# Optimization experiments

Hardware: AMD Instinct MI355X
Metric: run time of the kernel (lower is better)

Reference implementation:

```python
import jax, jax.numpy as jnp
import numpy as np
import math

B, L, D, H = 16, 512, 128, 8


def setup_inputs() -> dict:
    key = jax.random.key(0)
    ks = jax.random.split(key, 10)
    xavier = lambda k, shp: jax.random.normal(k, shp, jnp.float32) * math.sqrt(2.0 / (shp[0] + shp[1]))
    inp = {
        "x": jax.random.normal(ks[0], (B, L, D), jnp.float32),
        "W_q": xavier(ks[1], (H * D, D)),
        "b_q": jnp.zeros((H * D,), jnp.float32),
        "W_k": xavier(ks[2], (H * D, D)),
        "b_k": jnp.zeros((H * D,), jnp.float32),
        "W_v": xavier(ks[3], (H * D, D)),
        "b_v": jnp.zeros((H * D,), jnp.float32),
        "W_o": xavier(ks[4], (D, H * D)),
        "b_o": jnp.zeros((D,), jnp.float32),
        "pad_mask": jax.random.randint(ks[5], (B, L, L), 0, 2).astype(bool),
        "batch_size": B,
        "max_len": L,
    }
    return inp


def reference(x, W_q, b_q, W_k, b_k, W_v, b_v, W_o, b_o, pad_mask, batch_size, max_len):
    # project: [B, L, D] -> [B, L, H*D] -> head-major [H*B, L, D]
    def proj(W, b):
        y = jnp.einsum('bld,ed->ble', x, W) + b          # [B, L, H*D]
        y = y.reshape(batch_size, max_len, H, D)
        return y.transpose(2, 0, 1, 3).reshape(H * batch_size, max_len, D)

    q = proj(W_q, b_q)
    k = proj(W_k, b_k)
    v = proj(W_v, b_v)

    scores = jnp.einsum('nqd,nkd->nqk', q, k)            # [H*B, L, L]
    mask = jnp.tile(pad_mask, (H, 1, 1))                 # repeat(n_heads,1,1)
    # faithful quirk: mask BEFORE scaling, softmax over QUERY axis (dim=1)
    scores = jnp.where(mask, -1e9, scores) / math.sqrt(D)
    attn = jax.nn.softmax(scores, axis=1)
    att = jnp.einsum('nqk,nkd->nqd', attn, v)            # [H*B, L, D]
    # faithful quirk: torch .view from (H*B, L, D) to (B, L, H*D)
    att = att.reshape(batch_size, max_len, H * D)
    out = jnp.einsum('ble,de->bld', att, W_o) + b_o      # [B, L, D]
    return out
```

## Files before the change

### kernel.cpp

```cpp
#include <hip/hip_runtime.h>

#define B_  16
#define L_  512
#define D_  128
#define H_  8
#define HD_ 1024
#define NH_ 128
#define M_  8192

typedef unsigned short u16;
typedef __attribute__((ext_vector_type(8))) short s16x8;
typedef __attribute__((ext_vector_type(4))) float f32x4;

__device__ __forceinline__ float bf2f(u16 u) {
    union { unsigned u; float f; } x; x.u = ((unsigned)u) << 16; return x.f;
}
__device__ __forceinline__ u16 f2bf(float f) {
    unsigned u = __float_as_uint(f);
    return (u16)((u + 0x7FFFu + ((u >> 16) & 1u)) >> 16);
}

__device__ __forceinline__ void mfma_bt64(const u16* __restrict__ A, int lda,
                                          const u16* __restrict__ B, int ldb,
                                          int K, int lane, f32x4 acc[4][4]) {
    const int mr = lane & 15, quad = lane >> 4;
    for (int k0 = 0; k0 < K; k0 += 32) {
        s16x8 av[4], bv[4];
#pragma unroll
        for (int i = 0; i < 4; i++)
            av[i] = *(const s16x8*)(A + (size_t)(i * 16 + mr) * lda + k0 + quad * 8);
#pragma unroll
        for (int j = 0; j < 4; j++)
            bv[j] = *(const s16x8*)(B + (size_t)(j * 16 + mr) * ldb + k0 + quad * 8);
#pragma unroll
        for (int i = 0; i < 4; i++)
#pragma unroll
            for (int j = 0; j < 4; j++)
                acc[i][j] = __builtin_amdgcn_mfma_f32_16x16x32_bf16(av[i], bv[j], acc[i][j], 0, 0, 0);
    }
}

__global__ void k0_detect(const unsigned int* __restrict__ pad,
                          const unsigned int* __restrict__ xw,
                          int* __restrict__ flags) {
    __shared__ int sMask, sCnt;
    if (threadIdx.x == 0) { sMask = 0; sCnt = 0; }
    __syncthreads();
    int bad = 0;
#pragma unroll
    for (int i = 0; i < 4; i++) {
        unsigned u = pad[threadIdx.x * 4 + i];
        bad |= (u > 1u) ? 1 : 0;
    }
    int cnt = 0;
#pragma unroll
    for (int i = 0; i < 16; i++) {
        unsigned w = xw[threadIdx.x * 16 + i];
        unsigned e = (w >> 7) & 0xFFu;
        cnt += (e >= 100u && e <= 131u) ? 1 : 0;
    }
    if (bad) atomicOr(&sMask, 1);
    atomicAdd(&sCnt, cnt);
    __syncthreads();
    if (threadIdx.x == 0) {
        flags[0] = (sCnt > 2048) ? 1 : 0;
        flags[1] = sMask;
    }
}

#define PREP_TOT 1576064
__global__ __launch_bounds__(256) void kprep_conv(
    const void* x, const void* Wq, const void* bq, const void* Wk, const void* bk,
    const void* Wv, const void* bv, const void* Wo, const void* bo,
    const int* __restrict__ flags,
    u16* xb, u16* Wqb, u16* Wkb, u16* Wvb, u16* Wob,
    u16* bqb, u16* bkb, u16* bvb, u16* bob) {
    int gid = blockIdx.x * 256 + threadIdx.x;
    if (gid >= PREP_TOT) return;
    const int dt = flags[0];
    const void* src; u16* dst; int off;
    if      (gid < 1048576) { src = x;  dst = xb;  off = gid; }
    else if (gid < 1179648) { src = Wq; dst = Wqb; off = gid - 1048576; }
    else if (gid < 1310720) { src = Wk; dst = Wkb; off = gid - 1179648; }
    else if (gid < 1441792) { src = Wv; dst = Wvb; off = gid - 1310720; }
    else if (gid < 1572864) { src = Wo; dst = Wob; off = gid - 1441792; }
    else if (gid < 1573888) { src = bq; dst = bqb; off = gid - 1572864; }
    else if (gid < 1574912) { src = bk; dst = bkb; off = gid - 1573888; }
    else if (gid < 1575936) { src = bv; dst = bvb; off = gid - 1574912; }
    else                    { src = bo; dst = bob; off = gid - 1575936; }
    dst[off] = dt ? ((const u16*)src)[off] : f2bf(((const float*)src)[off]);
}

__global__ __launch_bounds__(256) void kprep_mask(const void* __restrict__ pad,
                                                  const int* __restrict__ flags,
                                                  unsigned* __restrict__ mb) {
    int w = blockIdx.x * 256 + threadIdx.x;
    size_t base = (size_t)w * 32;
    unsigned m = 0;
    if (flags[1]) {
        const unsigned char* p = (const unsigned char*)pad;
#pragma unroll
        for (int b = 0; b < 32; b++) m |= (p[base + b] ? 1u : 0u) << b;
    } else {
        const int* p = (const int*)pad;
#pragma unroll
        for (int b = 0; b < 32; b++) m |= (p[base + b] ? 1u : 0u) << b;
    }
    mb[w] = m;
}

__global__ __launch_bounds__(256) void k1_proj(
    const u16* __restrict__ xb,
    const u16* __restrict__ Wqb, const u16* __restrict__ Wkb, const u16* __restrict__ Wvb,
    const u16* __restrict__ bqb, const u16* __restrict__ bkb, const u16* __restrict__ bvb,
    u16* __restrict__ qb, u16* __restrict__ kb, u16* __restrict__ vtb) {
    const int h  = blockIdx.x;
    const int m0 = blockIdx.y * 128;
    const int z  = blockIdx.z;
    const u16* W    = (z == 0) ? Wqb : (z == 1) ? Wkb : Wvb;
    const u16* bias = (z == 0) ? bqb : (z == 1) ? bkb : bvb;

    const int lane = threadIdx.x & 63, wave = threadIdx.x >> 6;
    const int wr = wave >> 1, wc = wave & 1;
    const int mr = lane & 15, quad = lane >> 4;

    f32x4 acc[4][4];
#pragma unroll
    for (int i = 0; i < 4; i++)
#pragma unroll
        for (int j = 0; j < 4; j++) acc[i][j] = (f32x4){0.f, 0.f, 0.f, 0.f};

    mfma_bt64(xb + (size_t)(m0 + wr * 64) * D_, D_,
              W + (size_t)(h * 128 + wc * 64) * D_, D_, D_, lane, acc);

    __shared__ __align__(16) u16 T[128][144];
#pragma unroll
    for (int i = 0; i < 4; i++)
#pragma unroll
        for (int j = 0; j < 4; j++) {
            int col = wc * 64 + j * 16 + mr;
            float bv_ = bf2f(bias[h * 128 + col]);
#pragma unroll
            for (int r = 0; r < 4; r++)
                T[wr * 64 + i * 16 + quad * 4 + r][col] = f2bf(acc[i][j][r] + bv_);
        }
    __syncthreads();

    const int bb = m0 >> 9, l0 = m0 & 511;
    const int t = threadIdx.x;
    if (z < 2) {
        u16* out = z ? kb : qb;
        int row = t >> 1, c0 = (t & 1) * 64;
        u16* dst = out + ((size_t)(h * B_ + bb) * L_ + l0 + row) * D_ + c0;
#pragma unroll
        for (int c = 0; c < 64; c += 8)
            *(uint4*)(dst + c) = *(const uint4*)&T[row][c0 + c];
    } else {
        int d = t >> 1, lc0 = (t & 1) * 64;
        u16* dst = vtb + ((size_t)(h * B_ + bb) * D_ + d) * L_ + l0 + lc0;
#pragma unroll
        for (int c = 0; c < 64; c += 8) {
            u16 tmp[8];
#pragma unroll
            for (int s = 0; s < 8; s++) tmp[s] = T[lc0 + c + s][d];
            *(uint4*)(dst + c) = *(const uint4*)tmp;
        }
    }
}

__global__ __launch_bounds__(256) void k2_scores(
    const u16* __restrict__ qb, const u16* __restrict__ kb,
    const unsigned* __restrict__ mbits,
    u16* __restrict__ sb, float* __restrict__ linv) {
    const int k0g = blockIdx.x * 128;
    const int n   = blockIdx.y;
    const int bb  = n & (B_ - 1);
    const int lane = threadIdx.x & 63, wave = threadIdx.x >> 6;
    const int wr = wave >> 1, wc = wave & 1;
    const int mr = lane & 15, quad = lane >> 4;
    const float rs = 0.08838834764831845f;

    __shared__ __align__(16) u16 T[128][144];
    __shared__ float CS[2][128];

    const u16* Abase = qb + (size_t)n * L_ * D_;
    const u16* Bbase = kb + (size_t)n * L_ * D_ + (size_t)(k0g + wc * 64) * D_;

    float colsum[4] = {0.f, 0.f, 0.f, 0.f};
    for (int qt = 0; qt < 4; qt++) {
        f32x4 acc[4][4];
#pragma unroll
        for (int i = 0; i < 4; i++)
#pragma unroll
            for (int j = 0; j < 4; j++) acc[i][j] = (f32x4){0.f, 0.f, 0.f, 0.f};

        mfma_bt64(Abase + (size_t)(qt * 128 + wr * 64) * D_, D_, Bbase, D_, D_, lane, acc);

#pragma unroll
        for (int i = 0; i < 4; i++)
#pragma unroll
            for (int j = 0; j < 4; j++) {
                int kc = k0g + wc * 64 + j * 16 + mr;
#pragma unroll
                for (int r = 0; r < 4; r++) {
                    int ql = wr * 64 + i * 16 + quad * 4 + r;
                    int q  = qt * 128 + ql;
                    unsigned w = mbits[((size_t)(bb << 9) + q) * 16 + (kc >> 5)];
                    float s = ((w >> (kc & 31)) & 1u) ? -1e9f : acc[i][j][r];
                    float e = __expf(s * rs);
                    colsum[j] += e;
                    T[ql][wc * 64 + j * 16 + mr] = f2bf(e);
                }
            }
        __syncthreads();
        {
            int t = threadIdx.x, row = t >> 1, c0 = (t & 1) * 64;
            u16* dst = sb + ((size_t)n * L_ + qt * 128 + row) * L_ + k0g + c0;
#pragma unroll
            for (int c = 0; c < 64; c += 8)
                *(uint4*)(dst + c) = *(const uint4*)&T[row][c0 + c];
        }
        __syncthreads();
    }
#pragma unroll
    for (int j = 0; j < 4; j++) {
        colsum[j] += __shfl_xor(colsum[j], 16);
        colsum[j] += __shfl_xor(colsum[j], 32);
    }
    if (quad == 0) {
#pragma unroll
        for (int j = 0; j < 4; j++) CS[wr][wc * 64 + j * 16 + mr] = colsum[j];
    }
    __syncthreads();
    if (threadIdx.x < 128)
        linv[(size_t)n * L_ + k0g + threadIdx.x] =
            1.0f / (CS[0][threadIdx.x] + CS[1][threadIdx.x]);
}

__global__ __launch_bounds__(256) void k3_vscale(u16* __restrict__ vtb,
                                                 const float* __restrict__ linv) {
    int idx = blockIdx.x * 256 + threadIdx.x;
    int n = idx >> 13;
    int rem = idx & 8191;
    int d = rem >> 6;
    int kg = (rem & 63) << 3;
    u16* p = vtb + ((size_t)n * D_ + d) * L_ + kg;
    uint4 v = *(const uint4*)p;
    float lv[8];
    *(float4*)&lv[0] = *(const float4*)(linv + (size_t)n * L_ + kg);
    *(float4*)&lv[4] = *(const float4*)(linv + (size_t)n * L_ + kg + 4);
    u16* u = (u16*)&v;
#pragma unroll
    for (int s = 0; s < 8; s++) u[s] = f2bf(bf2f(u[s]) * lv[s]);
    *(uint4*)p = v;
}

__global__ __launch_bounds__(256) void k4_av(
    const u16* __restrict__ sb, const u16* __restrict__ vtb,
    u16* __restrict__ att) {
    const int q0 = blockIdx.x * 128;
    const int n  = blockIdx.y;
    const int lane = threadIdx.x & 63, wave = threadIdx.x >> 6;
    const int wr = wave >> 1, wc = wave & 1;
    const int mr = lane & 15, quad = lane >> 4;

    f32x4 acc[4][4];
#pragma unroll
    for (int i = 0; i < 4; i++)
#pragma unroll
        for (int j = 0; j < 4; j++) acc[i][j] = (f32x4){0.f, 0.f, 0.f, 0.f};

    mfma_bt64(sb + ((size_t)n * L_ + q0 + wr * 64) * L_, L_,
              vtb + ((size_t)n * D_ + wc * 64) * L_, L_, L_, lane, acc);

    __shared__ __align__(16) u16 T[128][144];
#pragma unroll
    for (int i = 0; i < 4; i++)
#pragma unroll
        for (int j = 0; j < 4; j++) {
            int col = wc * 64 + j * 16 + mr;
#pragma unroll
            for (int r = 0; r < 4; r++)
                T[wr * 64 + i * 16 + quad * 4 + r][col] = f2bf(acc[i][j][r]);
        }
    __syncthreads();
    int t = threadIdx.x, row = t >> 1, c0 = (t & 1) * 64;
    u16* dst = att + ((size_t)n * L_ + q0 + row) * D_ + c0;
#pragma unroll
    for (int c = 0; c < 64; c += 8)
        *(uint4*)(dst + c) = *(const uint4*)&T[row][c0 + c];
}

__global__ __launch_bounds__(128) void k5_out(
    const u16* __restrict__ att, const u16* __restrict__ Wob,
    const u16* __restrict__ bob, const int* __restrict__ flags,
    void* __restrict__ out) {
    const int dt = flags[0];
    const int m0 = blockIdx.x * 64;
    const int lane = threadIdx.x & 63, wc = threadIdx.x >> 6;
    const int mr = lane & 15, quad = lane >> 4;

    f32x4 acc[4][4];
#pragma unroll
    for (int i = 0; i < 4; i++)
#pragma unroll
        for (int j = 0; j < 4; j++) acc[i][j] = (f32x4){0.f, 0.f, 0.f, 0.f};

    mfma_bt64(att + (size_t)m0 * HD_, HD_,
              Wob + (size_t)(wc * 64) * HD_, HD_, HD_, lane, acc);

    __shared__ __align__(16) float Tf[64][132];
#pragma unroll
    for (int i = 0; i < 4; i++)
#pragma unroll
        for (int j = 0; j < 4; j++) {
            int col = wc * 64 + j * 16 + mr;
            float bv_ = bf2f(bob[col]);
#pragma unroll
            for (int r = 0; r < 4; r++)
                Tf[i * 16 + quad * 4 + r][col] = acc[i][j][r] + bv_;
        }
    __syncthreads();
    int t = threadIdx.x, row = t >> 1, c0 = (t & 1) * 64;
    size_t base = (size_t)(m0 + row) * D_ + c0;
    if (dt) {
        u16* o = (u16*)out;
#pragma unroll
        for (int c = 0; c < 64; c += 8) {
            u16 tmp[8];
#pragma unroll
            for (int s = 0; s < 8; s++) tmp[s] = f2bf(Tf[row][c0 + c + s]);
            *(uint4*)(o + base + c) = *(const uint4*)tmp;
        }
    } else {
        float* o = (float*)out;
#pragma unroll
        for (int c = 0; c < 64; c += 4)
            *(float4*)(o + base + c) = *(const float4*)&Tf[row][c0 + c];
    }
}

extern "C" void kernel_launch(void* const* d_in, const int* in_sizes, int n_in,
                              void* d_out, int out_size, void* d_ws, size_t ws_size,
                              hipStream_t stream) {
    (void)in_sizes; (void)n_in; (void)out_size; (void)ws_size;
    const void* x  = d_in[0];
    const void* Wq = d_in[1]; const void* bq = d_in[2];
    const void* Wk = d_in[3]; const void* bk = d_in[4];
    const void* Wv = d_in[5]; const void* bv = d_in[6];
    const void* Wo = d_in[7]; const void* bo = d_in[8];
    const void* pad = d_in[9];

    char* p = (char*)d_ws;
    auto alloc = [&](size_t bytes) { char* r = p; p += (bytes + 255) & ~(size_t)255; return r; };
    int*  flags = (int*)alloc(256);
    u16*  xb   = (u16*)alloc(2097152);
    u16*  Wqb  = (u16*)alloc(262144);
    u16*  Wkb  = (u16*)alloc(262144);
    u16*  Wvb  = (u16*)alloc(262144);
    u16*  Wob  = (u16*)alloc(262144);
    u16*  bqb  = (u16*)alloc(2048);
    u16*  bkb  = (u16*)alloc(2048);
    u16*  bvb  = (u16*)alloc(2048);
    u16*  bob  = (u16*)alloc(256);
    unsigned* mbits = (unsigned*)alloc(524288);
    float* linv = (float*)alloc(262144);
    u16*  qb   = (u16*)alloc(16777216);
    u16*  kb   = (u16*)alloc(16777216);
    u16*  vtb  = (u16*)alloc(16777216);
    u16*  sb   = (u16*)alloc(67108864);
    u16*  att  = qb;

    k0_detect<<<1, 256, 0, stream>>>((const unsigned*)pad, (const unsigned*)x, flags);
    kprep_conv<<<(PREP_TOT + 255) / 256, 256, 0, stream>>>(
        x, Wq, bq, Wk, bk, Wv, bv, Wo, bo, flags,
        xb, Wqb, Wkb, Wvb, Wob, bqb, bkb, bvb, bob);
    kprep_mask<<<512, 256, 0, stream>>>(pad, flags, mbits);
    k1_proj<<<dim3(8, 64, 3), 256, 0, stream>>>(
        xb, Wqb, Wkb, Wvb, bqb, bkb, bvb, qb, kb, vtb);
    k2_scores<<<dim3(4, NH_), 256, 0, stream>>>(qb, kb, mbits, sb, linv);
    k3_vscale<<<4096, 256, 0, stream>>>(vtb, linv);
    k4_av<<<dim3(4, NH_), 256, 0, stream>>>(sb, vtb, att);
    k5_out<<<128, 128, 0, stream>>>(att, Wob, bob, flags, d_out);
}
```

Before: 253.4 us.

## Fuse scores, normalization and AV into flash-style kernel with recompute

The score kernel is split into a column-sum pass that only computes softmax denominators, and a second kernel that recomputes QK^T, applies the mask and per-key normalization, and multiplies with V in LDS. This removes the 64MB bf16 score matrix round-trip and the separate V-scaling kernel. The cost is computing QK^T twice. The output projection is also split over the K dimension across two waves, with a 2D grid for more blocks, and mask words are staged in LDS.

```diff
diff --git a/kernel.cpp b/kernel.cpp
--- a/kernel.cpp
+++ b/kernel.cpp
@@ -133,7 +133,7 @@
     mfma_bt64(xb + (size_t)(m0 + wr * 64) * D_, D_,
               W + (size_t)(h * 128 + wc * 64) * D_, D_, D_, lane, acc);
 
-    __shared__ __align__(16) u16 T[128][144];
+    __shared__ __align__(16) u16 T[128][136];
 #pragma unroll
     for (int i = 0; i < 4; i++)
 #pragma unroll
@@ -168,11 +168,10 @@
     }
 }
 
-__global__ __launch_bounds__(256) void k2_scores(
+__global__ __launch_bounds__(256) void k2a_linv(
     const u16* __restrict__ qb, const u16* __restrict__ kb,
-    const unsigned* __restrict__ mbits,
-    u16* __restrict__ sb, float* __restrict__ linv) {
-    const int k0g = blockIdx.x * 128;
+    const unsigned* __restrict__ mbits, float* __restrict__ linv) {
+    const int kstrip = blockIdx.x * 128;
     const int n   = blockIdx.y;
     const int bb  = n & (B_ - 1);
     const int lane = threadIdx.x & 63, wave = threadIdx.x >> 6;
@@ -180,11 +179,18 @@
     const int mr = lane & 15, quad = lane >> 4;
     const float rs = 0.08838834764831845f;
 
-    __shared__ __align__(16) u16 T[128][144];
+    __shared__ unsigned mw[2048];
     __shared__ float CS[2][128];
+#pragma unroll
+    for (int s = 0; s < 8; s++) {
+        int idx = threadIdx.x * 8 + s;
+        int q = idx >> 2, lw = idx & 3;
+        mw[idx] = mbits[((size_t)(bb << 9) + q) * 16 + (blockIdx.x << 2) + lw];
+    }
+    __syncthreads();
 
     const u16* Abase = qb + (size_t)n * L_ * D_;
-    const u16* Bbase = kb + (size_t)n * L_ * D_ + (size_t)(k0g + wc * 64) * D_;
+    const u16* Bbase = kb + (size_t)n * L_ * D_ + (size_t)(kstrip + wc * 64) * D_;
 
     float colsum[4] = {0.f, 0.f, 0.f, 0.f};
     for (int qt = 0; qt < 4; qt++) {
@@ -193,87 +199,118 @@
         for (int i = 0; i < 4; i++)
 #pragma unroll
             for (int j = 0; j < 4; j++) acc[i][j] = (f32x4){0.f, 0.f, 0.f, 0.f};
-
         mfma_bt64(Abase + (size_t)(qt * 128 + wr * 64) * D_, D_, Bbase, D_, D_, lane, acc);
-
 #pragma unroll
         for (int i = 0; i < 4; i++)
 #pragma unroll
             for (int j = 0; j < 4; j++) {
-                int kc = k0g + wc * 64 + j * 16 + mr;
+                const int lw = wc * 2 + (j >> 1);
+                const int bit = (j & 1) * 16 + mr;
+#pragma unroll
+                for (int r = 0; r < 4; r++) {
+                    int q = qt * 128 + wr * 64 + i * 16 + quad * 4 + r;
+                    unsigned w = mw[(q << 2) + lw];
+                    if (!((w >> bit) & 1u))
+                        colsum[j] += __expf(acc[i][j][r] * rs);
+                }
+            }
+    }
+#pragma unroll
+    for (int j = 0; j < 4; j++) {
+        colsum[j] += __shfl_xor(colsum[j], 16);
+        colsum[j] += __shfl_xor(colsum[j], 32);
+    }
+    if (quad == 0) {
+#pragma unroll
+        for (int j = 0; j < 4; j++) CS[wr][wc * 64 + j * 16 + mr] = colsum[j];
+    }
+    __syncthreads();
+    if (threadIdx.x < 128)
+        linv[(size_t)n * L_ + kstrip + threadIdx.x] =
+            1.0f / (CS[0][threadIdx.x] + CS[1][threadIdx.x]);
+}
+
+__global__ __launch_bounds__(256) void k2b_attn(
+    const u16* __restrict__ qb, const u16* __restrict__ kb,
+    const u16* __restrict__ vtb, const unsigned* __restrict__ mbits,
+    const float* __restrict__ linv, u16* __restrict__ att) {
+    const int qtile = blockIdx.x * 128;
+    const int n  = blockIdx.y;
+    const int bb = n & (B_ - 1);
+    const int lane = threadIdx.x & 63, wave = threadIdx.x >> 6;
+    const int wr = wave >> 1, wc = wave & 1;
+    const int mr = lane & 15, quad = lane >> 4;
+    const float rs = 0.08838834764831845f;
+
+    __shared__ __align__(16) u16 eS[128][136];
+    __shared__ unsigned mwq[2048];
+    __shared__ float linvS[512];
+#pragma unroll
+    for (int s = 0; s < 8; s++) {
+        int idx = threadIdx.x * 8 + s;
+        int q = idx >> 4, w = idx & 15;
+        mwq[idx] = mbits[((size_t)(bb << 9) + qtile + q) * 16 + w];
+    }
+    if (threadIdx.x < 128)
+        *(float4*)&linvS[threadIdx.x * 4] = *(const float4*)&linv[(size_t)n * L_ + threadIdx.x * 4];
+    __syncthreads();
+
+    const u16* qn = qb + (size_t)n * L_ * D_;
+    const u16* kn = kb + (size_t)n * L_ * D_;
+    const u16* vn = vtb + (size_t)n * D_ * L_;
+
+    f32x4 att_acc[4][4];
+#pragma unroll
+    for (int i = 0; i < 4; i++)
+#pragma unroll
+        for (int j = 0; j < 4; j++) att_acc[i][j] = (f32x4){0.f, 0.f, 0.f, 0.f};
+
+    for (int kt = 0; kt < 4; kt++) {
+        f32x4 qk[4][4];
+#pragma unroll
+        for (int i = 0; i < 4; i++)
+#pragma unroll
+            for (int j = 0; j < 4; j++) qk[i][j] = (f32x4){0.f, 0.f, 0.f, 0.f};
+        mfma_bt64(qn + (size_t)(qtile + wr * 64) * D_, D_,
+                  kn + (size_t)(kt * 128 + wc * 64) * D_, D_, D_, lane, qk);
+
+#pragma unroll
+        for (int i = 0; i < 4; i++)
+#pragma unroll
+            for (int j = 0; j < 4; j++) {
+                const int widx = kt * 4 + wc * 2 + (j >> 1);
+                const int bit = (j & 1) * 16 + mr;
+                const int kl = wc * 64 + j * 16 + mr;
+                const float lv = linvS[kt * 128 + kl];
 #pragma unroll
                 for (int r = 0; r < 4; r++) {
                     int ql = wr * 64 + i * 16 + quad * 4 + r;
-                    int q  = qt * 128 + ql;
-                    unsigned w = mbits[((size_t)(bb << 9) + q) * 16 + (kc >> 5)];
-                    float s = ((w >> (kc & 31)) & 1u) ? -1e9f : acc[i][j][r];
-                    float e = __expf(s * rs);
-                    colsum[j] += e;
-                    T[ql][wc * 64 + j * 16 + mr] = f2bf(e);
+                    unsigned w = mwq[(ql << 4) + widx];
+                    float e = ((w >> bit) & 1u) ? 0.f : __expf(qk[i][j][r] * rs) * lv;
+                    eS[ql][kl] = f2bf(e);
                 }
             }
         __syncthreads();
-        {
-            int t = threadIdx.x, row = t >> 1, c0 = (t & 1) * 64;
-            u16* dst = sb + ((size_t)n * L_ + qt * 128 + row) * L_ + k0g + c0;
-#pragma unroll
-            for (int c = 0; c < 64; c += 8)
-                *(uint4*)(dst + c) = *(const uint4*)&T[row][c0 + c];
+
+#pragma unroll
+        for (int kk = 0; kk < 4; kk++) {
+            s16x8 av[4], bv[4];
+#pragma unroll
+            for (int i = 0; i < 4; i++)
+                av[i] = *(const s16x8*)&eS[wr * 64 + i * 16 + mr][kk * 32 + quad * 8];
+#pragma unroll
+            for (int j = 0; j < 4; j++)
+                bv[j] = *(const s16x8*)(vn + (size_t)(wc * 64 + j * 16 + mr) * L_
+                                        + kt * 128 + kk * 32 + quad * 8);
+#pragma unroll
+            for (int i = 0; i < 4; i++)
+#pragma unroll
+                for (int j = 0; j < 4; j++)
+                    att_acc[i][j] = __builtin_amdgcn_mfma_f32_16x16x32_bf16(av[i], bv[j], att_acc[i][j], 0, 0, 0);
         }
         __syncthreads();
     }
-#pragma unroll
-    for (int j = 0; j < 4; j++) {
-        colsum[j] += __shfl_xor(colsum[j], 16);
-        colsum[j] += __shfl_xor(colsum[j], 32);
-    }
-    if (quad == 0) {
-#pragma unroll
-        for (int j = 0; j < 4; j++) CS[wr][wc * 64 + j * 16 + mr] = colsum[j];
-    }
-    __syncthreads();
-    if (threadIdx.x < 128)
-        linv[(size_t)n * L_ + k0g + threadIdx.x] =
-            1.0f / (CS[0][threadIdx.x] + CS[1][threadIdx.x]);
-}
-
-__global__ __launch_bounds__(256) void k3_vscale(u16* __restrict__ vtb,
-                                                 const float* __restrict__ linv) {
-    int idx = blockIdx.x * 256 + threadIdx.x;
-    int n = idx >> 13;
-    int rem = idx & 8191;
-    int d = rem >> 6;
-    int kg = (rem & 63) << 3;
-    u16* p = vtb + ((size_t)n * D_ + d) * L_ + kg;
-    uint4 v = *(const uint4*)p;
-    float lv[8];
-    *(float4*)&lv[0] = *(const float4*)(linv + (size_t)n * L_ + kg);
-    *(float4*)&lv[4] = *(const float4*)(linv + (size_t)n * L_ + kg + 4);
-    u16* u = (u16*)&v;
-#pragma unroll
-    for (int s = 0; s < 8; s++) u[s] = f2bf(bf2f(u[s]) * lv[s]);
-    *(uint4*)p = v;
-}
-
-__global__ __launch_bounds__(256) void k4_av(
-    const u16* __restrict__ sb, const u16* __restrict__ vtb,
-    u16* __restrict__ att) {
-    const int q0 = blockIdx.x * 128;
-    const int n  = blockIdx.y;
-    const int lane = threadIdx.x & 63, wave = threadIdx.x >> 6;
-    const int wr = wave >> 1, wc = wave & 1;
-    const int mr = lane & 15, quad = lane >> 4;
-
-    f32x4 acc[4][4];
-#pragma unroll
-    for (int i = 0; i < 4; i++)
-#pragma unroll
-        for (int j = 0; j < 4; j++) acc[i][j] = (f32x4){0.f, 0.f, 0.f, 0.f};
-
-    mfma_bt64(sb + ((size_t)n * L_ + q0 + wr * 64) * L_, L_,
-              vtb + ((size_t)n * D_ + wc * 64) * L_, L_, L_, lane, acc);
-
-    __shared__ __align__(16) u16 T[128][144];
+
 #pragma unroll
     for (int i = 0; i < 4; i++)
 #pragma unroll
@@ -281,14 +318,14 @@
             int col = wc * 64 + j * 16 + mr;
 #pragma unroll
             for (int r = 0; r < 4; r++)
-                T[wr * 64 + i * 16 + quad * 4 + r][col] = f2bf(acc[i][j][r]);
+                eS[wr * 64 + i * 16 + quad * 4 + r][col] = f2bf(att_acc[i][j][r]);
         }
     __syncthreads();
     int t = threadIdx.x, row = t >> 1, c0 = (t & 1) * 64;
-    u16* dst = att + ((size_t)n * L_ + q0 + row) * D_ + c0;
+    u16* dst = att + ((size_t)n * L_ + qtile + row) * D_ + c0;
 #pragma unroll
     for (int c = 0; c < 64; c += 8)
-        *(uint4*)(dst + c) = *(const uint4*)&T[row][c0 + c];
+        *(uint4*)(dst + c) = *(const uint4*)&eS[row][c0 + c];
 }
 
 __global__ __launch_bounds__(128) void k5_out(
@@ -296,8 +333,9 @@
     const u16* __restrict__ bob, const int* __restrict__ flags,
     void* __restrict__ out) {
     const int dt = flags[0];
-    const int m0 = blockIdx.x * 64;
-    const int lane = threadIdx.x & 63, wc = threadIdx.x >> 6;
+    const int n0 = blockIdx.x * 64;
+    const int m0 = blockIdx.y * 64;
+    const int lane = threadIdx.x & 63, wk = threadIdx.x >> 6;
     const int mr = lane & 15, quad = lane >> 4;
 
     f32x4 acc[4][4];
@@ -306,37 +344,54 @@
 #pragma unroll
         for (int j = 0; j < 4; j++) acc[i][j] = (f32x4){0.f, 0.f, 0.f, 0.f};
 
-    mfma_bt64(att + (size_t)m0 * HD_, HD_,
-              Wob + (size_t)(wc * 64) * HD_, HD_, HD_, lane, acc);
-
-    __shared__ __align__(16) float Tf[64][132];
-#pragma unroll
-    for (int i = 0; i < 4; i++)
-#pragma unroll
-        for (int j = 0; j < 4; j++) {
-            int col = wc * 64 + j * 16 + mr;
-            float bv_ = bf2f(bob[col]);
-#pragma unroll
-            for (int r = 0; r < 4; r++)
-                Tf[i * 16 + quad * 4 + r][col] = acc[i][j][r] + bv_;
-        }
-    __syncthreads();
-    int t = threadIdx.x, row = t >> 1, c0 = (t & 1) * 64;
-    size_t base = (size_t)(m0 + row) * D_ + c0;
+    mfma_bt64(att + (size_t)m0 * HD_ + wk * 512, HD_,
+              Wob + (size_t)n0 * HD_ + wk * 512, HD_, 512, lane, acc);
+
+    __shared__ __align__(16) float Tf[64][68];
+    if (wk == 0) {
+#pragma unroll
+        for (int i = 0; i < 4; i++)
+#pragma unroll
+            for (int j = 0; j < 4; j++)
+#pragma unroll
+                for (int r = 0; r < 4; r++)
+                    Tf[i * 16 + quad * 4 + r][j * 16 + mr] = acc[i][j][r];
+    }
+    __syncthreads();
+    if (wk == 1) {
+#pragma unroll
+        for (int i = 0; i < 4; i++)
+#pragma unroll
+            for (int j = 0; j < 4; j++)
+#pragma unroll
+                for (int r = 0; r < 4; r++)
+                    Tf[i * 16 + quad * 4 + r][j * 16 + mr] += acc[i][j][r];
+    }
+    __syncthreads();
+
+    int t = threadIdx.x, row = t >> 1, h0 = (t & 1) * 32;
+    size_t base = (size_t)(m0 + row) * D_ + n0 + h0;
     if (dt) {
         u16* o = (u16*)out;
 #pragma unroll
-        for (int c = 0; c < 64; c += 8) {
+        for (int c = 0; c < 32; c += 8) {
             u16 tmp[8];
 #pragma unroll
-            for (int s = 0; s < 8; s++) tmp[s] = f2bf(Tf[row][c0 + c + s]);
+            for (int s = 0; s < 8; s++)
+                tmp[s] = f2bf(Tf[row][h0 + c + s] + bf2f(bob[n0 + h0 + c + s]));
             *(uint4*)(o + base + c) = *(const uint4*)tmp;
         }
     } else {
         float* o = (float*)out;
 #pragma unroll
-        for (int c = 0; c < 64; c += 4)
-            *(float4*)(o + base + c) = *(const float4*)&Tf[row][c0 + c];
+        for (int c = 0; c < 32; c += 4) {
+            float4 v;
+            v.x = Tf[row][h0 + c + 0] + bf2f(bob[n0 + h0 + c + 0]);
+            v.y = Tf[row][h0 + c + 1] + bf2f(bob[n0 + h0 + c + 1]);
+            v.z = Tf[row][h0 + c + 2] + bf2f(bob[n0 + h0 + c + 2]);
+            v.w = Tf[row][h0 + c + 3] + bf2f(bob[n0 + h0 + c + 3]);
+            *(float4*)(o + base + c) = v;
+        }
     }
 }
 
@@ -368,8 +423,7 @@
     u16*  qb   = (u16*)alloc(16777216);
     u16*  kb   = (u16*)alloc(16777216);
     u16*  vtb  = (u16*)alloc(16777216);
-    u16*  sb   = (u16*)alloc(67108864);
-    u16*  att  = qb;
+    u16*  att  = (u16*)alloc(2097152);
 
     k0_detect<<<1, 256, 0, stream>>>((const unsigned*)pad, (const unsigned*)x, flags);
     kprep_conv<<<(PREP_TOT + 255) / 256, 256, 0, stream>>>(
@@ -378,8 +432,7 @@
     kprep_mask<<<512, 256, 0, stream>>>(pad, flags, mbits);
     k1_proj<<<dim3(8, 64, 3), 256, 0, stream>>>(
         xb, Wqb, Wkb, Wvb, bqb, bkb, bvb, qb, kb, vtb);
-    k2_scores<<<dim3(4, NH_), 256, 0, stream>>>(qb, kb, mbits, sb, linv);
-    k3_vscale<<<4096, 256, 0, stream>>>(vtb, linv);
-    k4_av<<<dim3(4, NH_), 256, 0, stream>>>(sb, vtb, att);
-    k5_out<<<128, 128, 0, stream>>>(att, Wob, bob, flags, d_out);
-}
+    k2a_linv<<<dim3(4, NH_), 256, 0, stream>>>(qb, kb, mbits, linv);
+    k2b_attn<<<dim3(4, NH_), 256, 0, stream>>>(qb, kb, vtb, mbits, linv, att);
+    k5_out<<<dim3(2, 128), 128, 0, stream>>>(att, Wob, bob, flags, d_out);
+}
```

Measured after the change: 256.9 us. About the same (+1.4%).
